# Performance work log

Hardware: AMD Instinct MI355X
Metric: run time of the kernel (lower is better)

## Reference

```python
import jax, jax.numpy as jnp
import numpy as np

N_SRC = [700000, 51200, 5120]
N_DST = [51200, 5120, 1024]
N_EDGE = [768000, 51200, 5120]
IN_FEATS, N_HIDDEN, N_CLASSES = 128, 256, 47


def setup_inputs() -> dict:
    key = jax.random.key(0)
    ks = jax.random.split(key, 16)
    inp = {}
    inp["x"] = jax.random.normal(ks[0], (N_SRC[0], IN_FEATS), dtype=jnp.float32)
    # edge lists per block: src indexes block-src nodes, dst indexes block-dst nodes
    for l in range(3):
        inp[f"src{l}"] = jax.random.randint(ks[1 + 2 * l], (N_EDGE[l],), 0, N_SRC[l], dtype=jnp.int32)
        inp[f"dst{l}"] = jax.random.randint(ks[2 + 2 * l], (N_EDGE[l],), 0, N_DST[l], dtype=jnp.int32)
    dims = [(IN_FEATS, N_HIDDEN), (N_HIDDEN, N_HIDDEN), (N_HIDDEN, N_CLASSES)]
    for l, (di, do) in enumerate(dims):
        scale = 1.0 / np.sqrt(di)
        inp[f"Ws{l}"] = jax.random.normal(ks[7 + 3 * l], (di, do), dtype=jnp.float32) * scale
        inp[f"Wn{l}"] = jax.random.normal(ks[8 + 3 * l], (di, do), dtype=jnp.float32) * scale
        inp[f"b{l}"] = jnp.zeros((do,), dtype=jnp.float32)
    return inp


def _sage_conv(h, src, dst, n_dst, Ws, Wn, b):
    # mean-aggregate neighbor (src) features onto dst nodes, then dual linear
    h_dst = h[:n_dst]                                   # dst nodes are a prefix of src nodes
    msg = jax.ops.segment_sum(h[src], dst, num_segments=n_dst)
    deg = jax.ops.segment_sum(jnp.ones((src.shape[0], 1), h.dtype), dst, num_segments=n_dst)
    h_neigh = msg / jnp.maximum(deg, 1.0)               # zero-degree dst -> 0 (DGL convention)
    return h_dst @ Ws + h_neigh @ Wn + b


def reference(x, src0, dst0, src1, dst1, src2, dst2,
              Ws0, Wn0, b0, Ws1, Wn1, b1, Ws2, Wn2, b2):
    h = _sage_conv(x, src0, dst0, N_DST[0], Ws0, Wn0, b0)
    h = jax.nn.relu(h)  # dropout = identity in eval
    h = _sage_conv(h, src1, dst1, N_DST[1], Ws1, Wn1, b1)
    h = jax.nn.relu(h)
    h = _sage_conv(h, src2, dst2, N_DST[2], Ws2, Wn2, b2)
    return h
```

## Files before the change

kernel.cpp:

```cpp
#include <hip/hip_runtime.h>


typedef __bf16 bf16x8 __attribute__((ext_vector_type(8)));
typedef float f32x4 __attribute__((ext_vector_type(4)));

static __device__ __forceinline__ unsigned short f32_to_bf16(float f) {
    unsigned u = __float_as_uint(f);
    u += 0x7fffu + ((u >> 16) & 1u);
    return (unsigned short)(u >> 16);
}


__global__ void hist_kernel(const int* __restrict__ dst, int* __restrict__ counts, int n_edge) {
    int i = blockIdx.x * 256 + threadIdx.x;
    if (i < n_edge) atomicAdd(&counts[dst[i]], 1);
}

__global__ void scan_kernel(const int* __restrict__ counts, int* __restrict__ offsets,
                            int* __restrict__ cursor, int n) {
    __shared__ int wsum[4];
    __shared__ int s_carry;
    if (threadIdx.x == 0) s_carry = 0;
    __syncthreads();
    const int lane = threadIdx.x & 63;
    const int wid = threadIdx.x >> 6;
    for (int base = 0; base < n; base += 2048) {
        int idx = base + threadIdx.x * 8;
        int v[8];
#pragma unroll
        for (int u = 0; u < 8; ++u) v[u] = (idx + u < n) ? counts[idx + u] : 0;
        int tsum = 0;
#pragma unroll
        for (int u = 0; u < 8; ++u) { int t = v[u]; v[u] = tsum; tsum += t; }
        int incl = tsum;
#pragma unroll
        for (int d = 1; d < 64; d <<= 1) {
            int t = __shfl_up(incl, d, 64);
            if (lane >= d) incl += t;
        }
        int wexcl = incl - tsum;
        if (lane == 63) wsum[wid] = incl;
        __syncthreads();
        int wbase = 0;
        for (int w = 0; w < wid; ++w) wbase += wsum[w];
        int carry = s_carry;
        int pre = carry + wbase + wexcl;
#pragma unroll
        for (int u = 0; u < 8; ++u)
            if (idx + u < n) { int o = pre + v[u]; offsets[idx + u] = o; cursor[idx + u] = o; }
        __syncthreads();
        if (threadIdx.x == 0) s_carry = carry + wsum[0] + wsum[1] + wsum[2] + wsum[3];
        __syncthreads();
    }
    if (threadIdx.x == 0) offsets[n] = s_carry;
}

__global__ void fill_kernel(const int* __restrict__ src, const int* __restrict__ dst,
                            int* __restrict__ cursor, int* __restrict__ csr_src, int n_edge) {
    int i = blockIdx.x * 256 + threadIdx.x;
    if (i < n_edge) {
        int pos = atomicAdd(&cursor[dst[i]], 1);
        csr_src[pos] = src[i];
    }
}


__global__ void gather_f32_128(const float* __restrict__ h, const int* __restrict__ csr_src,
                               const int* __restrict__ offsets, unsigned short* __restrict__ out,
                               int n_dst) {
    int row = (blockIdx.x * blockDim.x + threadIdx.x) >> 6;
    if (row >= n_dst) return;
    int lane = threadIdx.x & 63;
    int beg = offsets[row], end = offsets[row + 1];
    const float2* hp = (const float2*)h;
    float ax = 0.f, ay = 0.f;
    int i = beg;
    for (; i + 1 < end; i += 2) {
        int s0 = csr_src[i], s1 = csr_src[i + 1];
        float2 v0 = hp[(size_t)s0 * 64 + lane];
        float2 v1 = hp[(size_t)s1 * 64 + lane];
        ax += v0.x + v1.x; ay += v0.y + v1.y;
    }
    if (i < end) {
        int s = csr_src[i];
        float2 v = hp[(size_t)s * 64 + lane];
        ax += v.x; ay += v.y;
    }
    float inv = 1.0f / fmaxf((float)(end - beg), 1.0f);
    unsigned pack = (unsigned)f32_to_bf16(ax * inv) | ((unsigned)f32_to_bf16(ay * inv) << 16);
    ((unsigned*)out)[(size_t)row * 64 + lane] = pack;
}

__global__ void gather_bf16_256(const unsigned short* __restrict__ h, const int* __restrict__ csr_src,
                                const int* __restrict__ offsets, unsigned short* __restrict__ out,
                                int n_dst) {
    int row = (blockIdx.x * blockDim.x + threadIdx.x) >> 6;
    if (row >= n_dst) return;
    int lane = threadIdx.x & 63;
    int beg = offsets[row], end = offsets[row + 1];
    const uint2* hp = (const uint2*)h;
    float a0 = 0.f, a1 = 0.f, a2 = 0.f, a3 = 0.f;
    int i = beg;
    for (; i + 1 < end; i += 2) {
        int s0 = csr_src[i], s1 = csr_src[i + 1];
        uint2 u0 = hp[(size_t)s0 * 64 + lane];
        uint2 u1 = hp[(size_t)s1 * 64 + lane];
        a0 += __uint_as_float(u0.x << 16) + __uint_as_float(u1.x << 16);
        a1 += __uint_as_float(u0.x & 0xffff0000u) + __uint_as_float(u1.x & 0xffff0000u);
        a2 += __uint_as_float(u0.y << 16) + __uint_as_float(u1.y << 16);
        a3 += __uint_as_float(u0.y & 0xffff0000u) + __uint_as_float(u1.y & 0xffff0000u);
    }
    if (i < end) {
        int s = csr_src[i];
        uint2 u = hp[(size_t)s * 64 + lane];
        a0 += __uint_as_float(u.x << 16);
        a1 += __uint_as_float(u.x & 0xffff0000u);
        a2 += __uint_as_float(u.y << 16);
        a3 += __uint_as_float(u.y & 0xffff0000u);
    }
    float inv = 1.0f / fmaxf((float)(end - beg), 1.0f);
    uint2 o;
    o.x = (unsigned)f32_to_bf16(a0 * inv) | ((unsigned)f32_to_bf16(a1 * inv) << 16);
    o.y = (unsigned)f32_to_bf16(a2 * inv) | ((unsigned)f32_to_bf16(a3 * inv) << 16);
    ((uint2*)out)[(size_t)row * 64 + lane] = o;
}


__global__ void cast_f32_bf16(const float* __restrict__ in, unsigned short* __restrict__ out, int n4) {
    int i = blockIdx.x * 256 + threadIdx.x;
    if (i >= n4) return;
    float4 v = ((const float4*)in)[i];
    uint2 o;
    o.x = (unsigned)f32_to_bf16(v.x) | ((unsigned)f32_to_bf16(v.y) << 16);
    o.y = (unsigned)f32_to_bf16(v.z) | ((unsigned)f32_to_bf16(v.w) << 16);
    ((uint2*)out)[i] = o;
}

__global__ void build_wcatT(const float* __restrict__ Ws, const float* __restrict__ Wn,
                            unsigned short* __restrict__ WT, int K1, int N, int kshift) {
    int idx = blockIdx.x * 256 + threadIdx.x;
    int Ktot = 1 << kshift;
    if (idx >= (N << kshift)) return;
    int n = idx >> kshift;
    int k = idx & (Ktot - 1);
    float v = (k < K1) ? Ws[(size_t)k * N + n] : Wn[(size_t)(k - K1) * N + n];
    WT[idx] = f32_to_bf16(v);
}

template <int RELU, int OUT_BF16>
__launch_bounds__(256)
__global__ void sage_gemm_mfma(const unsigned short* __restrict__ Hdst,
                               const unsigned short* __restrict__ Hneigh,
                               const unsigned short* __restrict__ WT,
                               const float* __restrict__ bias,
                               void* __restrict__ Out,
                               int N, int K1) {
    const int Ktot = 2 * K1;
    __shared__ unsigned short As[64][56];
    __shared__ unsigned short Bs[64][56];

    const int t = threadIdx.x;
    const int lane = t & 63;
    const int w = t >> 6;
    const int wm = (w >> 1) * 32;
    const int wn = (w & 1) * 32;
    const int bm = blockIdx.y * 64;
    const int bn = blockIdx.x * 64;

    const int ldr = t >> 2;
    const int ldk = (t & 3) * 8;

    f32x4 acc[2][2] = {};

    const int ktiles = Ktot >> 5;
    for (int kt = 0; kt < ktiles; ++kt) {
        const int k0 = kt << 5;
        {
            const unsigned short* base = (k0 < K1)
                ? (Hdst + (size_t)(bm + ldr) * K1 + k0 + ldk)
                : (Hneigh + (size_t)(bm + ldr) * K1 + (k0 - K1) + ldk);
            *(uint4*)&As[ldr][ldk] = *(const uint4*)base;
        }
        {
            int n = bn + ldr;
            uint4 v = {0, 0, 0, 0};
            if (n < N) v = *(const uint4*)(WT + (size_t)n * Ktot + k0 + ldk);
            *(uint4*)&Bs[ldr][ldk] = v;
        }
        __syncthreads();

        const int fr = lane & 15;
        const int fk = (lane >> 4) * 8;
        bf16x8 a0 = *(const bf16x8*)&As[wm + fr][fk];
        bf16x8 a1 = *(const bf16x8*)&As[wm + 16 + fr][fk];
        bf16x8 b0 = *(const bf16x8*)&Bs[wn + fr][fk];
        bf16x8 b1 = *(const bf16x8*)&Bs[wn + 16 + fr][fk];
        acc[0][0] = __builtin_amdgcn_mfma_f32_16x16x32_bf16(a0, b0, acc[0][0], 0, 0, 0);
        acc[0][1] = __builtin_amdgcn_mfma_f32_16x16x32_bf16(a0, b1, acc[0][1], 0, 0, 0);
        acc[1][0] = __builtin_amdgcn_mfma_f32_16x16x32_bf16(a1, b0, acc[1][0], 0, 0, 0);
        acc[1][1] = __builtin_amdgcn_mfma_f32_16x16x32_bf16(a1, b1, acc[1][1], 0, 0, 0);
        __syncthreads();
    }

    const int quad = lane >> 4;
    const int colL = lane & 15;
#pragma unroll
    for (int mt = 0; mt < 2; ++mt)
#pragma unroll
        for (int nt = 0; nt < 2; ++nt)
#pragma unroll
            for (int r = 0; r < 4; ++r) {
                int grow = bm + wm + mt * 16 + quad * 4 + r;
                int gcol = bn + wn + nt * 16 + colL;
                if (gcol < N) {
                    float v = acc[mt][nt][r] + bias[gcol];
                    if (RELU) v = fmaxf(v, 0.0f);
                    if (OUT_BF16) ((unsigned short*)Out)[(size_t)grow * N + gcol] = f32_to_bf16(v);
                    else ((float*)Out)[(size_t)grow * N + gcol] = v;
                }
            }
}


extern "C" void kernel_launch(void* const* d_in, const int* in_sizes, int n_in,
                              void* d_out, int out_size, void* d_ws, size_t ws_size,
                              hipStream_t stream) {
    const float* x    = (const float*)d_in[0];
    const int* src0 = (const int*)d_in[1];
    const int* dst0 = (const int*)d_in[2];
    const int* src1 = (const int*)d_in[3];
    const int* dst1 = (const int*)d_in[4];
    const int* src2 = (const int*)d_in[5];
    const int* dst2 = (const int*)d_in[6];
    const float* Ws0 = (const float*)d_in[7];
    const float* Wn0 = (const float*)d_in[8];
    const float* b0  = (const float*)d_in[9];
    const float* Ws1 = (const float*)d_in[10];
    const float* Wn1 = (const float*)d_in[11];
    const float* b1  = (const float*)d_in[12];
    const float* Ws2 = (const float*)d_in[13];
    const float* Wn2 = (const float*)d_in[14];
    const float* b2  = (const float*)d_in[15];
    float* out = (float*)d_out;

    char* ws = (char*)d_ws;
    unsigned short* xcast   = (unsigned short*)(ws + 0);
    unsigned short* h1      = (unsigned short*)(ws + 13107200);
    unsigned short* h2      = (unsigned short*)(ws + 39321600);
    unsigned short* hneigh0 = (unsigned short*)(ws + 41943040);
    unsigned short* hneigh1 = (unsigned short*)(ws + 55050240);
    unsigned short* hneigh2 = (unsigned short*)(ws + 57671680);
    unsigned short* WT0     = (unsigned short*)(ws + 58195968);
    unsigned short* WT1     = (unsigned short*)(ws + 58327040);
    unsigned short* WT2     = (unsigned short*)(ws + 58589184);
    int* counts  = (int*)(ws + 58637312);
    int* offsets = (int*)(ws + 58842112);
    int* cursor  = (int*)(ws + 59046928);
    int* csr0    = (int*)(ws + 59251728);
    int* csr1    = (int*)(ws + 62323728);
    int* csr2    = (int*)(ws + 62528528);

    cast_f32_bf16<<<(51200 * 128 / 4 + 255) / 256, 256, 0, stream>>>(x, xcast, 51200 * 128 / 4);
    build_wcatT<<<(256 * 256 + 255) / 256, 256, 0, stream>>>(Ws0, Wn0, WT0, 128, 256, 8);
    build_wcatT<<<(256 * 512 + 255) / 256, 256, 0, stream>>>(Ws1, Wn1, WT1, 256, 256, 9);
    build_wcatT<<<(47 * 512 + 255) / 256, 256, 0, stream>>>(Ws2, Wn2, WT2, 256, 47, 9);

    hipMemsetAsync(counts, 0, 51200 * 4, stream);
    hist_kernel<<<(768000 + 255) / 256, 256, 0, stream>>>(dst0, counts, 768000);
    scan_kernel<<<1, 256, 0, stream>>>(counts, offsets, cursor, 51200);
    fill_kernel<<<(768000 + 255) / 256, 256, 0, stream>>>(src0, dst0, cursor, csr0, 768000);
    gather_f32_128<<<(51200 * 64) / 256, 256, 0, stream>>>(x, csr0, offsets, hneigh0, 51200);
    {
        dim3 grid(4, 800);
        sage_gemm_mfma<1, 1><<<grid, 256, 0, stream>>>(xcast, hneigh0, WT0, b0, h1, 256, 128);
    }

    hipMemsetAsync(counts, 0, 5120 * 4, stream);
    hist_kernel<<<(51200 + 255) / 256, 256, 0, stream>>>(dst1, counts, 51200);
    scan_kernel<<<1, 256, 0, stream>>>(counts, offsets, cursor, 5120);
    fill_kernel<<<(51200 + 255) / 256, 256, 0, stream>>>(src1, dst1, cursor, csr1, 51200);
    gather_bf16_256<<<(5120 * 64) / 256, 256, 0, stream>>>(h1, csr1, offsets, hneigh1, 5120);
    {
        dim3 grid(4, 80);
        sage_gemm_mfma<1, 1><<<grid, 256, 0, stream>>>(h1, hneigh1, WT1, b1, h2, 256, 256);
    }

    hipMemsetAsync(counts, 0, 1024 * 4, stream);
    hist_kernel<<<(5120 + 255) / 256, 256, 0, stream>>>(dst2, counts, 5120);
    scan_kernel<<<1, 256, 0, stream>>>(counts, offsets, cursor, 1024);
    fill_kernel<<<(5120 + 255) / 256, 256, 0, stream>>>(src2, dst2, cursor, csr2, 5120);
    gather_bf16_256<<<(1024 * 64) / 256, 256, 0, stream>>>(h2, csr2, offsets, hneigh2, 1024);
    {
        dim3 grid(1, 16);
        sage_gemm_mfma<0, 0><<<grid, 256, 0, stream>>>(h2, hneigh2, WT2, b2, out, 47, 256);
    }
}
```

Measured before the change: 775.0 us.

## Batch graph-prep kernels across layers, widen gathers, and enlarge GEMM M-tile

Fuses the cast, weight transpose and count zeroing into one prep kernel, and merges the histogram, scan and fill steps for all three layers into single launches so layers 1 and 2 no longer run CSR construction serially. Gathers now have each half-wave handle alternate edges with 16-byte loads and combine the halves by shuffle. The GEMM tile grows to 128 rows with four M fragments per wave. This cuts launch count and per-launch overhead, and raises memory-level parallelism in the gather, at the cost of more registers and fewer GEMM blocks on the small layers.

```diff
diff --git a/kernel.cpp b/kernel.cpp
--- a/kernel.cpp
+++ b/kernel.cpp
@@ -9,23 +9,72 @@
     u += 0x7fffu + ((u >> 16) & 1u);
     return (unsigned short)(u >> 16);
 }
-
-
-__global__ void hist_kernel(const int* __restrict__ dst, int* __restrict__ counts, int n_edge) {
-    int i = blockIdx.x * 256 + threadIdx.x;
-    if (i < n_edge) atomicAdd(&counts[dst[i]], 1);
-}
-
-__global__ void scan_kernel(const int* __restrict__ counts, int* __restrict__ offsets,
-                            int* __restrict__ cursor, int n) {
-    __shared__ int wsum[4];
+static __device__ __forceinline__ float bf16lo(unsigned u) { return __uint_as_float(u << 16); }
+static __device__ __forceinline__ float bf16hi(unsigned u) { return __uint_as_float(u & 0xffff0000u); }
+
+__global__ void sage_prep(const float* __restrict__ x, unsigned short* __restrict__ xcast,
+                          const float* __restrict__ Ws0, const float* __restrict__ Wn0,
+                          const float* __restrict__ Ws1, const float* __restrict__ Wn1,
+                          const float* __restrict__ Ws2, const float* __restrict__ Wn2,
+                          unsigned short* __restrict__ WT0, unsigned short* __restrict__ WT1,
+                          unsigned short* __restrict__ WT2, int* __restrict__ counts) {
+    const int b = blockIdx.x;
+    if (b < 6400) {
+        int i = b * 256 + threadIdx.x;
+        float4 v = ((const float4*)x)[i];
+        uint2 o;
+        o.x = (unsigned)f32_to_bf16(v.x) | ((unsigned)f32_to_bf16(v.y) << 16);
+        o.y = (unsigned)f32_to_bf16(v.z) | ((unsigned)f32_to_bf16(v.w) << 16);
+        ((uint2*)xcast)[i] = o;
+    } else if (b < 6656) {
+        int idx = (b - 6400) * 256 + threadIdx.x;
+        int n = idx >> 8, k = idx & 255;
+        float v = (k < 128) ? Ws0[(size_t)k * 256 + n] : Wn0[(size_t)(k - 128) * 256 + n];
+        WT0[idx] = f32_to_bf16(v);
+    } else if (b < 7168) {
+        int idx = (b - 6656) * 256 + threadIdx.x;
+        int n = idx >> 9, k = idx & 511;
+        float v = (k < 256) ? Ws1[(size_t)k * 256 + n] : Wn1[(size_t)(k - 256) * 256 + n];
+        WT1[idx] = f32_to_bf16(v);
+    } else if (b < 7262) {
+        int idx = (b - 7168) * 256 + threadIdx.x;
+        int n = idx >> 9, k = idx & 511;
+        float v = (k < 256) ? Ws2[(size_t)k * 47 + n] : Wn2[(size_t)(k - 256) * 47 + n];
+        WT2[idx] = f32_to_bf16(v);
+    } else {
+        int i = (b - 7262) * 256 + threadIdx.x;
+        ((int4*)counts)[i] = make_int4(0, 0, 0, 0);
+    }
+}
+
+__global__ void sage_hist(const int* __restrict__ d0, int* __restrict__ c0,
+                          const int* __restrict__ d1, int* __restrict__ c1,
+                          const int* __restrict__ d2, int* __restrict__ c2) {
+    const int b = blockIdx.x;
+    if (b < 3000)       atomicAdd(&c0[d0[b * 256 + threadIdx.x]], 1);
+    else if (b < 3200)  atomicAdd(&c1[d1[(b - 3000) * 256 + threadIdx.x]], 1);
+    else                atomicAdd(&c2[d2[(b - 3200) * 256 + threadIdx.x]], 1);
+}
+
+__global__ void sage_scan(const int* __restrict__ c0, int* __restrict__ o0, int* __restrict__ u0,
+                          const int* __restrict__ c1, int* __restrict__ o1, int* __restrict__ u1,
+                          const int* __restrict__ c2, int* __restrict__ o2, int* __restrict__ u2) {
+    const int* counts; int* offsets; int* cursor; int n;
+    if (blockIdx.x == 0)      { counts = c0; offsets = o0; cursor = u0; n = 51200; }
+    else if (blockIdx.x == 1) { counts = c1; offsets = o1; cursor = u1; n = 5120; }
+    else                      { counts = c2; offsets = o2; cursor = u2; n = 1024; }
+
+    __shared__ int wsum[16];
+    __shared__ int wbase[16];
     __shared__ int s_carry;
-    if (threadIdx.x == 0) s_carry = 0;
+    const int tid = threadIdx.x;
+    const int lane = tid & 63;
+    const int wid = tid >> 6;
+    if (tid == 0) s_carry = 0;
     __syncthreads();
-    const int lane = threadIdx.x & 63;
-    const int wid = threadIdx.x >> 6;
-    for (int base = 0; base < n; base += 2048) {
-        int idx = base + threadIdx.x * 8;
+
+    for (int base = 0; base < n; base += 8192) {
+        int idx = base + tid * 8;
         int v[8];
 #pragma unroll
         for (int u = 0; u < 8; ++u) v[u] = (idx + u < n) ? counts[idx + u] : 0;
@@ -41,171 +90,191 @@
         int wexcl = incl - tsum;
         if (lane == 63) wsum[wid] = incl;
         __syncthreads();
-        int wbase = 0;
-        for (int w = 0; w < wid; ++w) wbase += wsum[w];
         int carry = s_carry;
-        int pre = carry + wbase + wexcl;
+        __syncthreads();
+        if (tid < 64) {
+            int s = (lane < 16) ? wsum[lane] : 0;
+            int inc = s;
+#pragma unroll
+            for (int d = 1; d < 16; d <<= 1) {
+                int t = __shfl_up(inc, d, 64);
+                if (lane >= d) inc += t;
+            }
+            if (lane < 16) wbase[lane] = carry + inc - s;
+            if (lane == 15) s_carry = carry + inc;
+        }
+        __syncthreads();
+        int pre = wbase[wid] + wexcl;
 #pragma unroll
         for (int u = 0; u < 8; ++u)
             if (idx + u < n) { int o = pre + v[u]; offsets[idx + u] = o; cursor[idx + u] = o; }
         __syncthreads();
-        if (threadIdx.x == 0) s_carry = carry + wsum[0] + wsum[1] + wsum[2] + wsum[3];
-        __syncthreads();
-    }
-    if (threadIdx.x == 0) offsets[n] = s_carry;
-}
-
-__global__ void fill_kernel(const int* __restrict__ src, const int* __restrict__ dst,
-                            int* __restrict__ cursor, int* __restrict__ csr_src, int n_edge) {
-    int i = blockIdx.x * 256 + threadIdx.x;
-    if (i < n_edge) {
-        int pos = atomicAdd(&cursor[dst[i]], 1);
-        csr_src[pos] = src[i];
-    }
-}
-
-
-__global__ void gather_f32_128(const float* __restrict__ h, const int* __restrict__ csr_src,
-                               const int* __restrict__ offsets, unsigned short* __restrict__ out,
-                               int n_dst) {
-    int row = (blockIdx.x * blockDim.x + threadIdx.x) >> 6;
+    }
+    if (tid == 0) offsets[n] = s_carry;
+}
+
+__global__ void sage_fill(const int* __restrict__ s0, const int* __restrict__ d0,
+                          int* __restrict__ u0, int* __restrict__ r0,
+                          const int* __restrict__ s1, const int* __restrict__ d1,
+                          int* __restrict__ u1, int* __restrict__ r1,
+                          const int* __restrict__ s2, const int* __restrict__ d2,
+                          int* __restrict__ u2, int* __restrict__ r2) {
+    const int b = blockIdx.x;
+    if (b < 3000) {
+        int i = b * 256 + threadIdx.x;
+        int pos = atomicAdd(&u0[d0[i]], 1);
+        r0[pos] = s0[i];
+    } else if (b < 3200) {
+        int i = (b - 3000) * 256 + threadIdx.x;
+        int pos = atomicAdd(&u1[d1[i]], 1);
+        r1[pos] = s1[i];
+    } else {
+        int i = (b - 3200) * 256 + threadIdx.x;
+        int pos = atomicAdd(&u2[d2[i]], 1);
+        r2[pos] = s2[i];
+    }
+}
+
+__global__ void sage_gather0(const float* __restrict__ x, const int* __restrict__ csr,
+                             const int* __restrict__ off, unsigned short* __restrict__ out,
+                             int n_dst) {
+    int row = (blockIdx.x * 256 + threadIdx.x) >> 6;
     if (row >= n_dst) return;
-    int lane = threadIdx.x & 63;
-    int beg = offsets[row], end = offsets[row + 1];
-    const float2* hp = (const float2*)h;
-    float ax = 0.f, ay = 0.f;
+    const int lane = threadIdx.x & 63;
+    const int half = lane >> 5;
+    const int fl = lane & 31;
+    const int beg = off[row], end = off[row + 1];
+    const float4* hp = (const float4*)x;
+    float4 acc = make_float4(0.f, 0.f, 0.f, 0.f);
     int i = beg;
     for (; i + 1 < end; i += 2) {
-        int s0 = csr_src[i], s1 = csr_src[i + 1];
-        float2 v0 = hp[(size_t)s0 * 64 + lane];
-        float2 v1 = hp[(size_t)s1 * 64 + lane];
-        ax += v0.x + v1.x; ay += v0.y + v1.y;
-    }
-    if (i < end) {
-        int s = csr_src[i];
-        float2 v = hp[(size_t)s * 64 + lane];
-        ax += v.x; ay += v.y;
-    }
-    float inv = 1.0f / fmaxf((float)(end - beg), 1.0f);
-    unsigned pack = (unsigned)f32_to_bf16(ax * inv) | ((unsigned)f32_to_bf16(ay * inv) << 16);
-    ((unsigned*)out)[(size_t)row * 64 + lane] = pack;
-}
-
-__global__ void gather_bf16_256(const unsigned short* __restrict__ h, const int* __restrict__ csr_src,
-                                const int* __restrict__ offsets, unsigned short* __restrict__ out,
-                                int n_dst) {
-    int row = (blockIdx.x * blockDim.x + threadIdx.x) >> 6;
+        int s = csr[i + half];
+        float4 v = hp[(size_t)s * 32 + fl];
+        acc.x += v.x; acc.y += v.y; acc.z += v.z; acc.w += v.w;
+    }
+    if (i < end && half == 0) {
+        int s = csr[i];
+        float4 v = hp[(size_t)s * 32 + fl];
+        acc.x += v.x; acc.y += v.y; acc.z += v.z; acc.w += v.w;
+    }
+    acc.x += __shfl_down(acc.x, 32);
+    acc.y += __shfl_down(acc.y, 32);
+    acc.z += __shfl_down(acc.z, 32);
+    acc.w += __shfl_down(acc.w, 32);
+    if (half == 0) {
+        float inv = 1.0f / fmaxf((float)(end - beg), 1.0f);
+        uint2 o;
+        o.x = (unsigned)f32_to_bf16(acc.x * inv) | ((unsigned)f32_to_bf16(acc.y * inv) << 16);
+        o.y = (unsigned)f32_to_bf16(acc.z * inv) | ((unsigned)f32_to_bf16(acc.w * inv) << 16);
+        ((uint2*)out)[(size_t)row * 32 + fl] = o;
+    }
+}
+
+__global__ void sage_gather256(const unsigned short* __restrict__ h, const int* __restrict__ csr,
+                               const int* __restrict__ off, unsigned short* __restrict__ out,
+                               int n_dst) {
+    int row = (blockIdx.x * 256 + threadIdx.x) >> 6;
     if (row >= n_dst) return;
-    int lane = threadIdx.x & 63;
-    int beg = offsets[row], end = offsets[row + 1];
-    const uint2* hp = (const uint2*)h;
-    float a0 = 0.f, a1 = 0.f, a2 = 0.f, a3 = 0.f;
+    const int lane = threadIdx.x & 63;
+    const int half = lane >> 5;
+    const int fl = lane & 31;
+    const int beg = off[row], end = off[row + 1];
+    const uint4* hp = (const uint4*)h;
+    float a[8] = {0.f, 0.f, 0.f, 0.f, 0.f, 0.f, 0.f, 0.f};
     int i = beg;
     for (; i + 1 < end; i += 2) {
-        int s0 = csr_src[i], s1 = csr_src[i + 1];
-        uint2 u0 = hp[(size_t)s0 * 64 + lane];
-        uint2 u1 = hp[(size_t)s1 * 64 + lane];
-        a0 += __uint_as_float(u0.x << 16) + __uint_as_float(u1.x << 16);
-        a1 += __uint_as_float(u0.x & 0xffff0000u) + __uint_as_float(u1.x & 0xffff0000u);
-        a2 += __uint_as_float(u0.y << 16) + __uint_as_float(u1.y << 16);
-        a3 += __uint_as_float(u0.y & 0xffff0000u) + __uint_as_float(u1.y & 0xffff0000u);
-    }
-    if (i < end) {
-        int s = csr_src[i];
-        uint2 u = hp[(size_t)s * 64 + lane];
-        a0 += __uint_as_float(u.x << 16);
-        a1 += __uint_as_float(u.x & 0xffff0000u);
-        a2 += __uint_as_float(u.y << 16);
-        a3 += __uint_as_float(u.y & 0xffff0000u);
-    }
-    float inv = 1.0f / fmaxf((float)(end - beg), 1.0f);
-    uint2 o;
-    o.x = (unsigned)f32_to_bf16(a0 * inv) | ((unsigned)f32_to_bf16(a1 * inv) << 16);
-    o.y = (unsigned)f32_to_bf16(a2 * inv) | ((unsigned)f32_to_bf16(a3 * inv) << 16);
-    ((uint2*)out)[(size_t)row * 64 + lane] = o;
-}
-
-
-__global__ void cast_f32_bf16(const float* __restrict__ in, unsigned short* __restrict__ out, int n4) {
-    int i = blockIdx.x * 256 + threadIdx.x;
-    if (i >= n4) return;
-    float4 v = ((const float4*)in)[i];
-    uint2 o;
-    o.x = (unsigned)f32_to_bf16(v.x) | ((unsigned)f32_to_bf16(v.y) << 16);
-    o.y = (unsigned)f32_to_bf16(v.z) | ((unsigned)f32_to_bf16(v.w) << 16);
-    ((uint2*)out)[i] = o;
-}
-
-__global__ void build_wcatT(const float* __restrict__ Ws, const float* __restrict__ Wn,
-                            unsigned short* __restrict__ WT, int K1, int N, int kshift) {
-    int idx = blockIdx.x * 256 + threadIdx.x;
-    int Ktot = 1 << kshift;
-    if (idx >= (N << kshift)) return;
-    int n = idx >> kshift;
-    int k = idx & (Ktot - 1);
-    float v = (k < K1) ? Ws[(size_t)k * N + n] : Wn[(size_t)(k - K1) * N + n];
-    WT[idx] = f32_to_bf16(v);
+        int s = csr[i + half];
+        uint4 u = hp[(size_t)s * 32 + fl];
+        a[0] += bf16lo(u.x); a[1] += bf16hi(u.x);
+        a[2] += bf16lo(u.y); a[3] += bf16hi(u.y);
+        a[4] += bf16lo(u.z); a[5] += bf16hi(u.z);
+        a[6] += bf16lo(u.w); a[7] += bf16hi(u.w);
+    }
+    if (i < end && half == 0) {
+        int s = csr[i];
+        uint4 u = hp[(size_t)s * 32 + fl];
+        a[0] += bf16lo(u.x); a[1] += bf16hi(u.x);
+        a[2] += bf16lo(u.y); a[3] += bf16hi(u.y);
+        a[4] += bf16lo(u.z); a[5] += bf16hi(u.z);
+        a[6] += bf16lo(u.w); a[7] += bf16hi(u.w);
+    }
+#pragma unroll
+    for (int k = 0; k < 8; ++k) a[k] += __shfl_down(a[k], 32);
+    if (half == 0) {
+        float inv = 1.0f / fmaxf((float)(end - beg), 1.0f);
+        uint4 o;
+        o.x = (unsigned)f32_to_bf16(a[0] * inv) | ((unsigned)f32_to_bf16(a[1] * inv) << 16);
+        o.y = (unsigned)f32_to_bf16(a[2] * inv) | ((unsigned)f32_to_bf16(a[3] * inv) << 16);
+        o.z = (unsigned)f32_to_bf16(a[4] * inv) | ((unsigned)f32_to_bf16(a[5] * inv) << 16);
+        o.w = (unsigned)f32_to_bf16(a[6] * inv) | ((unsigned)f32_to_bf16(a[7] * inv) << 16);
+        ((uint4*)out)[(size_t)row * 32 + fl] = o;
+    }
 }
 
 template <int RELU, int OUT_BF16>
 __launch_bounds__(256)
-__global__ void sage_gemm_mfma(const unsigned short* __restrict__ Hdst,
-                               const unsigned short* __restrict__ Hneigh,
-                               const unsigned short* __restrict__ WT,
-                               const float* __restrict__ bias,
-                               void* __restrict__ Out,
-                               int N, int K1) {
+__global__ void sage_gemm(const unsigned short* __restrict__ Hdst,
+                          const unsigned short* __restrict__ Hneigh,
+                          const unsigned short* __restrict__ WT,
+                          const float* __restrict__ bias,
+                          void* __restrict__ Out,
+                          int N, int K1) {
     const int Ktot = 2 * K1;
-    __shared__ unsigned short As[64][56];
-    __shared__ unsigned short Bs[64][56];
+    __shared__ unsigned short As[128][40];
+    __shared__ unsigned short Bs[64][40];
 
     const int t = threadIdx.x;
     const int lane = t & 63;
     const int w = t >> 6;
-    const int wm = (w >> 1) * 32;
+    const int wm = (w >> 1) * 64;
     const int wn = (w & 1) * 32;
-    const int bm = blockIdx.y * 64;
+    const int bm = blockIdx.y * 128;
     const int bn = blockIdx.x * 64;
 
-    const int ldr = t >> 2;
-    const int ldk = (t & 3) * 8;
-
-    f32x4 acc[2][2] = {};
+    const int rowA = t >> 1;
+    const int kA = (t & 1) * 16;
+    const int rowB = t >> 2;
+    const int kB = (t & 3) * 8;
+
+    f32x4 acc[4][2] = {};
 
     const int ktiles = Ktot >> 5;
     for (int kt = 0; kt < ktiles; ++kt) {
         const int k0 = kt << 5;
         {
-            const unsigned short* base = (k0 < K1)
-                ? (Hdst + (size_t)(bm + ldr) * K1 + k0 + ldk)
-                : (Hneigh + (size_t)(bm + ldr) * K1 + (k0 - K1) + ldk);
-            *(uint4*)&As[ldr][ldk] = *(const uint4*)base;
+            const unsigned short* src = (k0 < K1)
+                ? (Hdst + (size_t)(bm + rowA) * K1 + k0 + kA)
+                : (Hneigh + (size_t)(bm + rowA) * K1 + (k0 - K1) + kA);
+            uint4 va = *(const uint4*)src;
+            uint4 vb = *(const uint4*)(src + 8);
+            *(uint4*)&As[rowA][kA] = va;
+            *(uint4*)&As[rowA][kA + 8] = vb;
         }
         {
-            int n = bn + ldr;
+            int n = bn + rowB;
             uint4 v = {0, 0, 0, 0};
-            if (n < N) v = *(const uint4*)(WT + (size_t)n * Ktot + k0 + ldk);
-            *(uint4*)&Bs[ldr][ldk] = v;
+            if (n < N) v = *(const uint4*)(WT + (size_t)n * Ktot + k0 + kB);
+            *(uint4*)&Bs[rowB][kB] = v;
         }
         __syncthreads();
 
         const int fr = lane & 15;
         const int fk = (lane >> 4) * 8;
-        bf16x8 a0 = *(const bf16x8*)&As[wm + fr][fk];
-        bf16x8 a1 = *(const bf16x8*)&As[wm + 16 + fr][fk];
         bf16x8 b0 = *(const bf16x8*)&Bs[wn + fr][fk];
         bf16x8 b1 = *(const bf16x8*)&Bs[wn + 16 + fr][fk];
-        acc[0][0] = __builtin_amdgcn_mfma_f32_16x16x32_bf16(a0, b0, acc[0][0], 0, 0, 0);
-        acc[0][1] = __builtin_amdgcn_mfma_f32_16x16x32_bf16(a0, b1, acc[0][1], 0, 0, 0);
-        acc[1][0] = __builtin_amdgcn_mfma_f32_16x16x32_bf16(a1, b0, acc[1][0], 0, 0, 0);
-        acc[1][1] = __builtin_amdgcn_mfma_f32_16x16x32_bf16(a1, b1, acc[1][1], 0, 0, 0);
+#pragma unroll
+        for (int mt = 0; mt < 4; ++mt) {
+            bf16x8 am = *(const bf16x8*)&As[wm + mt * 16 + fr][fk];
+            acc[mt][0] = __builtin_amdgcn_mfma_f32_16x16x32_bf16(am, b0, acc[mt][0], 0, 0, 0);
+            acc[mt][1] = __builtin_amdgcn_mfma_f32_16x16x32_bf16(am, b1, acc[mt][1], 0, 0, 0);
+        }
         __syncthreads();
     }
 
     const int quad = lane >> 4;
     const int colL = lane & 15;
 #pragma unroll
-    for (int mt = 0; mt < 2; ++mt)
+    for (int mt = 0; mt < 4; ++mt)
 #pragma unroll
         for (int nt = 0; nt < 2; ++nt)
 #pragma unroll
@@ -253,45 +322,33 @@
     unsigned short* WT0     = (unsigned short*)(ws + 58195968);
     unsigned short* WT1     = (unsigned short*)(ws + 58327040);
     unsigned short* WT2     = (unsigned short*)(ws + 58589184);
-    int* counts  = (int*)(ws + 58637312);
-    int* offsets = (int*)(ws + 58842112);
-    int* cursor  = (int*)(ws + 59046928);
-    int* csr0    = (int*)(ws + 59251728);
-    int* csr1    = (int*)(ws + 62323728);
-    int* csr2    = (int*)(ws + 62528528);
-
-    cast_f32_bf16<<<(51200 * 128 / 4 + 255) / 256, 256, 0, stream>>>(x, xcast, 51200 * 128 / 4);
-    build_wcatT<<<(256 * 256 + 255) / 256, 256, 0, stream>>>(Ws0, Wn0, WT0, 128, 256, 8);
-    build_wcatT<<<(256 * 512 + 255) / 256, 256, 0, stream>>>(Ws1, Wn1, WT1, 256, 256, 9);
-    build_wcatT<<<(47 * 512 + 255) / 256, 256, 0, stream>>>(Ws2, Wn2, WT2, 256, 47, 9);
-
-    hipMemsetAsync(counts, 0, 51200 * 4, stream);
-    hist_kernel<<<(768000 + 255) / 256, 256, 0, stream>>>(dst0, counts, 768000);
-    scan_kernel<<<1, 256, 0, stream>>>(counts, offsets, cursor, 51200);
-    fill_kernel<<<(768000 + 255) / 256, 256, 0, stream>>>(src0, dst0, cursor, csr0, 768000);
-    gather_f32_128<<<(51200 * 64) / 256, 256, 0, stream>>>(x, csr0, offsets, hneigh0, 51200);
-    {
-        dim3 grid(4, 800);
-        sage_gemm_mfma<1, 1><<<grid, 256, 0, stream>>>(xcast, hneigh0, WT0, b0, h1, 256, 128);
-    }
-
-    hipMemsetAsync(counts, 0, 5120 * 4, stream);
-    hist_kernel<<<(51200 + 255) / 256, 256, 0, stream>>>(dst1, counts, 51200);
-    scan_kernel<<<1, 256, 0, stream>>>(counts, offsets, cursor, 5120);
-    fill_kernel<<<(51200 + 255) / 256, 256, 0, stream>>>(src1, dst1, cursor, csr1, 51200);
-    gather_bf16_256<<<(5120 * 64) / 256, 256, 0, stream>>>(h1, csr1, offsets, hneigh1, 5120);
-    {
-        dim3 grid(4, 80);
-        sage_gemm_mfma<1, 1><<<grid, 256, 0, stream>>>(h1, hneigh1, WT1, b1, h2, 256, 256);
-    }
-
-    hipMemsetAsync(counts, 0, 1024 * 4, stream);
-    hist_kernel<<<(5120 + 255) / 256, 256, 0, stream>>>(dst2, counts, 5120);
-    scan_kernel<<<1, 256, 0, stream>>>(counts, offsets, cursor, 1024);
-    fill_kernel<<<(5120 + 255) / 256, 256, 0, stream>>>(src2, dst2, cursor, csr2, 5120);
-    gather_bf16_256<<<(1024 * 64) / 256, 256, 0, stream>>>(h2, csr2, offsets, hneigh2, 1024);
-    {
-        dim3 grid(1, 16);
-        sage_gemm_mfma<0, 0><<<grid, 256, 0, stream>>>(h2, hneigh2, WT2, b2, out, 47, 256);
-    }
-}
+    int* counts0 = (int*)(ws + 58637312);
+    int* counts1 = (int*)(ws + 58842112);
+    int* counts2 = (int*)(ws + 58862592);
+    int* off0    = (int*)(ws + 58866688);
+    int* off1    = (int*)(ws + 59071504);
+    int* off2    = (int*)(ws + 59092000);
+    int* cur0    = (int*)(ws + 59096112);
+    int* cur1    = (int*)(ws + 59300912);
+    int* cur2    = (int*)(ws + 59321392);
+    int* csr0    = (int*)(ws + 59325488);
+    int* csr1    = (int*)(ws + 62397488);
+    int* csr2    = (int*)(ws + 62602288);
+
+    sage_prep<<<7318, 256, 0, stream>>>(x, xcast, Ws0, Wn0, Ws1, Wn1, Ws2, Wn2,
+                                        WT0, WT1, WT2, counts0);
+    sage_hist<<<3220, 256, 0, stream>>>(dst0, counts0, dst1, counts1, dst2, counts2);
+    sage_scan<<<3, 1024, 0, stream>>>(counts0, off0, cur0, counts1, off1, cur1, counts2, off2, cur2);
+    sage_fill<<<3220, 256, 0, stream>>>(src0, dst0, cur0, csr0,
+                                        src1, dst1, cur1, csr1,
+                                        src2, dst2, cur2, csr2);
+
+    sage_gather0<<<12800, 256, 0, stream>>>(x, csr0, off0, hneigh0, 51200);
+    { dim3 g(4, 400); sage_gemm<1, 1><<<g, 256, 0, stream>>>(xcast, hneigh0, WT0, b0, h1, 256, 128); }
+
+    sage_gather256<<<1280, 256, 0, stream>>>(h1, csr1, off1, hneigh1, 5120);
+    { dim3 g(4, 40); sage_gemm<1, 1><<<g, 256, 0, stream>>>(h1, hneigh1, WT1, b1, h2, 256, 256); }
+
+    sage_gather256<<<256, 256, 0, stream>>>(h2, csr2, off2, hneigh2, 1024);
+    { dim3 g(1, 8); sage_gemm<0, 0><<<g, 256, 0, stream>>>(h2, hneigh2, WT2, b2, out, 47, 256); }
+}
```

New measurement: 744.3 us. -4.0%, faster.
